# Optimization experiments

Hardware: AMD Instinct MI355X
Metric: run time of the kernel (lower is better)

The kernel has to match this reference:

```python
import jax, jax.numpy as jnp
import numpy as np

DIST_THRESHOLD = 0.1  # distance_threshold from __init__
NO_CODE_ID = -1


def setup_inputs() -> dict:
    key = jax.random.key(0)
    k1, k2 = jax.random.split(key)
    x = jax.random.normal(k1, (16, 4096, 64), dtype=jnp.float32)
    codes = jax.random.normal(k2, (4096, 64), dtype=jnp.float32)  # active codebook rows
    return {"x": x, "codes": codes}


def reference(x, codes):
    # Squared Euclidean distance (cdist ** 2) via the expansion
    x2 = jnp.sum(x * x, axis=-1, keepdims=True)            # [B, N, 1]
    c2 = jnp.sum(codes * codes, axis=-1)                    # [M]
    d2 = x2 + c2 - 2.0 * jnp.einsum("bnd,md->bnm", x, codes)  # [B, N, M]
    within = jnp.any(d2 <= DIST_THRESHOLD, axis=-1)         # [B, N]
    nn_ids = jnp.argmin(d2, axis=-1)                        # [B, N]
    return jnp.where(within, nn_ids, NO_CODE_ID)
```

## Files before the change

### kernel.cpp

```cpp
#include <hip/hip_runtime.h>
#include <stdint.h>

typedef float f32x4 __attribute__((ext_vector_type(4)));
typedef __bf16 bf16x8 __attribute__((ext_vector_type(8)));
typedef __bf16 bf16x4 __attribute__((ext_vector_type(4)));

#define NROWS 65536
#define NCODES 4096
#define NDIM 64
#define NSPLIT 4
#define STEPS 32
#define SSTEP 2
#define PHASES (STEPS / SSTEP)
#define BIAS 2048.0f
#define STRIPE_BYTES 131072u
#define STRIPE_MASK 0x1FFFFu


__device__ __forceinline__ void gld_lds16(const void* g, void* l) {
  __builtin_amdgcn_global_load_lds(
      (const __attribute__((address_space(1))) unsigned int*)g,
      (__attribute__((address_space(3))) unsigned int*)l, 16, 0, 0);
}

__device__ __forceinline__ uint32_t umin2(uint32_t a, uint32_t b) {
  return a < b ? a : b;
}

__global__ __launch_bounds__(256) void prep_codes_k(const float* __restrict__ codes,
                                                    float* __restrict__ nc2p,
                                                    __bf16* __restrict__ cb) {
  const int t = blockIdx.x * 256 + threadIdx.x;
  f32x4 v = *(const f32x4*)(codes + t * 4);
  bf16x4 o;
  float s = 0.f;
#pragma unroll
  for (int j = 0; j < 4; j++) {
    o[j] = (__bf16)v[j];
    s += v[j] * v[j];
  }
  *(bf16x4*)(cb + t * 4) = o;
  s += __shfl_xor(s, 1);
  s += __shfl_xor(s, 2);
  s += __shfl_xor(s, 4);
  s += __shfl_xor(s, 8);
  if ((threadIdx.x & 15) == 0) {
    const int c = t >> 4;
    const int pidx = (c >> 10) * 512 + ((c >> 5) & 31) * 16 + (c & 15);
    const int half = (c >> 4) & 1;
    nc2p[pidx * 2 + half] = -0.5f * s - BIAS;
  }
}

__global__ __launch_bounds__(256, 6) void nn_main(const float* __restrict__ x,
                                                  const __bf16* __restrict__ cbv,
                                                  const float2* __restrict__ nc2p,
                                                  uint32_t* __restrict__ karr,
                                                  float* __restrict__ x2arr) {
  const int tid  = threadIdx.x;
  const int lane = tid & 63;
  const int w    = tid >> 6;
  const int col  = lane & 15;
  const int quad = lane >> 4;
  const int stripe = blockIdx.x >> 9;
  const int rowgrp = blockIdx.x & 511;
  const int rowbase = rowgrp * 128 + w * 32;
  const int s0 = rowgrp & 31;
  const char* cbb = (const char*)cbv;

  __shared__ __align__(16) char stage[2][SSTEP * 4096];
  __shared__ __align__(8) float2 ncl[512];

  const uint32_t schunk = ((uint32_t)(tid * 16)) ^ ((((uint32_t)tid >> 3) & 7u) << 4);
  const char* srcbase = cbb + (uint32_t)stripe * STRIPE_BYTES + schunk;
  const uint32_t rot = (uint32_t)s0 * 4096u;
  gld_lds16((const char*)nc2p + stripe * 4096 + tid * 16, (char*)ncl + w * 1024);
#pragma unroll
  for (int i = 0; i < SSTEP; i++)
    gld_lds16(srcbase + ((rot + i * 4096u) & STRIPE_MASK),
              &stage[0][i * 4096 + w * 1024]);

  bf16x8 a[2][2];
  float x2part[2];
#pragma unroll
  for (int rt = 0; rt < 2; rt++) {
    const float* xr = x + (rowbase + rt * 16 + col) * NDIM + quad * 8;
    float p = 0.f;
#pragma unroll
    for (int kc = 0; kc < 2; kc++) {
      f32x4 v0 = *(const f32x4*)(xr + kc * 32);
      f32x4 v1 = *(const f32x4*)(xr + kc * 32 + 4);
      bf16x8 af;
#pragma unroll
      for (int j = 0; j < 4; j++) {
        af[j]     = (__bf16)v0[j];
        af[j + 4] = (__bf16)v1[j];
        p += v0[j] * v0[j] + v1[j] * v1[j];
      }
      a[rt][kc] = af;
    }
    x2part[rt] = p;
  }
#pragma unroll
  for (int rt = 0; rt < 2; rt++) {
    float p = x2part[rt];
    p += __shfl_xor(p, 16);
    p += __shfl_xor(p, 32);
    x2part[rt] = p;
  }
  if (stripe == 0 && quad == 0) {
#pragma unroll
    for (int rt = 0; rt < 2; rt++) x2arr[rowbase + rt * 16 + col] = x2part[rt];
  }

  uint32_t bestK[2][4];
#pragma unroll
  for (int rt = 0; rt < 2; rt++)
#pragma unroll
    for (int j = 0; j < 4; j++) bestK[rt][j] = 0xFFFFFFFFu;

  const uint32_t swz = ((uint32_t)(col & 7)) << 4;
  const uint32_t o00 = ((uint32_t)(col * 128 + quad * 16)) ^ swz;
  const uint32_t o01 = ((uint32_t)(col * 128 + 64 + quad * 16)) ^ swz;
  const uint32_t o10 = ((uint32_t)(2048 + col * 128 + quad * 16)) ^ swz;
  const uint32_t o11 = ((uint32_t)(2048 + col * 128 + 64 + quad * 16)) ^ swz;

  __syncthreads();

#pragma unroll 1
  for (int p = 0; p < PHASES; ++p) {
    if (p < PHASES - 1) {
      const uint32_t pb = rot + (uint32_t)(p + 1) * (SSTEP * 4096u);
      char* dst = &stage[(p + 1) & 1][w * 1024];
#pragma unroll
      for (int i = 0; i < SSTEP; i++)
        gld_lds16(srcbase + ((pb + i * 4096u) & STRIPE_MASK), dst + i * 4096);
    }
    const char* sb = stage[p & 1];
#pragma unroll
    for (int ss = 0; ss < SSTEP; ss++) {
      const int s_eff = (s0 + p * SSTEP + ss) & 31;
      const float2 nv = ncl[s_eff * 16 + col];
      bf16x8 b00 = *(const bf16x8*)(sb + ss * 4096 + o00);
      bf16x8 b01 = *(const bf16x8*)(sb + ss * 4096 + o01);
      bf16x8 b10 = *(const bf16x8*)(sb + ss * 4096 + o10);
      bf16x8 b11 = *(const bf16x8*)(sb + ss * 4096 + o11);
      f32x4 ci0 = {nv.x, nv.x, nv.x, nv.x};
      f32x4 ci1 = {nv.y, nv.y, nv.y, nv.y};
      const uint32_t vk0 = (uint32_t)(col | (s_eff << 5));
      const uint32_t vk1 = vk0 | 16u;
#pragma unroll
      for (int rt = 0; rt < 2; rt++) {
        f32x4 acc0 = __builtin_amdgcn_mfma_f32_16x16x32_bf16(a[rt][0], b00, ci0, 0, 0, 0);
        acc0 = __builtin_amdgcn_mfma_f32_16x16x32_bf16(a[rt][1], b01, acc0, 0, 0, 0);
        f32x4 acc1 = __builtin_amdgcn_mfma_f32_16x16x32_bf16(a[rt][0], b10, ci1, 0, 0, 0);
        acc1 = __builtin_amdgcn_mfma_f32_16x16x32_bf16(a[rt][1], b11, acc1, 0, 0, 0);
#pragma unroll
        for (int j = 0; j < 4; j++) {
          const uint32_t k0 = (__builtin_bit_cast(uint32_t, acc0[j]) & 0xFFFFFC00u) | vk0;
          const uint32_t k1 = (__builtin_bit_cast(uint32_t, acc1[j]) & 0xFFFFFC00u) | vk1;
          bestK[rt][j] = umin2(bestK[rt][j], umin2(k0, k1));
        }
      }
    }
    __syncthreads();
  }

#pragma unroll
  for (int rt = 0; rt < 2; rt++) {
#pragma unroll
    for (int j = 0; j < 4; j++) {
      uint32_t bk = bestK[rt][j];
#pragma unroll
      for (int off = 1; off < 16; off <<= 1) {
        const uint32_t ok = (uint32_t)__shfl_xor((int)bk, off);
        bk = umin2(bk, ok);
      }
      if (col == 0) {
        const int row = rowbase + rt * 16 + quad * 4 + j;
        karr[stripe * NROWS + row] = bk;
      }
    }
  }
}

__global__ __launch_bounds__(256) void nn_final(const uint32_t* __restrict__ karr,
                                                const float* __restrict__ x2arr,
                                                int* __restrict__ out) {
  const int row = blockIdx.x * blockDim.x + threadIdx.x;
  if (row >= NROWS) return;
  uint32_t best = karr[row];
  int bs = 0;
#pragma unroll
  for (int s = 1; s < NSPLIT; s++) {
    const uint32_t kk = karr[s * NROWS + row];
    if (kk < best) {
      best = kk;
      bs = s;
    }
  }
  const float Tp = __builtin_bit_cast(float, best & 0xFFFFFC00u);
  const float d2 = fmaf(-2.0f, Tp, x2arr[row]) - 2.0f * BIAS;
  out[row] = (d2 <= 0.1f) ? (bs * 1024 + (int)(best & 1023u)) : -1;
}

extern "C" void kernel_launch(void* const* d_in, const int* in_sizes, int n_in,
                              void* d_out, int out_size, void* d_ws, size_t ws_size,
                              hipStream_t stream) {
  const float* x = (const float*)d_in[0];
  const float* codes = (const float*)d_in[1];
  int* out = (int*)d_out;

  char* ws = (char*)d_ws;
  __bf16* cb = (__bf16*)ws;
  float* nc2p = (float*)(ws + 0x080000);
  uint32_t* karr = (uint32_t*)(ws + 0x100000);
  float* x2arr = (float*)(ws + 0x300000);

  prep_codes_k<<<256, 256, 0, stream>>>(codes, nc2p, cb);
  nn_main<<<2048, 256, 0, stream>>>(x, cb, (const float2*)nc2p, karr, x2arr);
  nn_final<<<256, 256, 0, stream>>>(karr, x2arr, out);
}
```

Baseline: 98.63 us.

## Drop codebook split across blocks and fuse final reduction into main kernel

Each block now scans all 4096 codes instead of one of four 1024-code stripes, so the grid shrinks from 2048 to 512 blocks. The threshold test and output write move into the main kernel, which removes the nn_final launch and the karr/x2arr workspace round trip. The packed key now keeps 12 index bits, so 2 fewer distance mantissa bits survive, slightly coarsening tie-breaking. With 512 blocks of 256 threads there may be too little parallelism to fill the GPU, and each block runs a loop four times longer.

Result: no change. 99.28 us (+0.7%).

```diff
diff --git a/kernel.cpp b/kernel.cpp
--- a/kernel.cpp
+++ b/kernel.cpp
@@ -8,13 +8,11 @@
 #define NROWS 65536
 #define NCODES 4096
 #define NDIM 64
-#define NSPLIT 4
-#define STEPS 32
+#define STEPS 128
 #define SSTEP 2
 #define PHASES (STEPS / SSTEP)
 #define BIAS 2048.0f
-#define STRIPE_BYTES 131072u
-#define STRIPE_MASK 0x1FFFFu
+#define CBMASK 0x7FFFF
 
 
 __device__ __forceinline__ void gld_lds16(const void* g, void* l) {
@@ -46,7 +44,7 @@
   s += __shfl_xor(s, 8);
   if ((threadIdx.x & 15) == 0) {
     const int c = t >> 4;
-    const int pidx = (c >> 10) * 512 + ((c >> 5) & 31) * 16 + (c & 15);
+    const int pidx = (c >> 5) * 16 + (c & 15);
     const int half = (c >> 4) & 1;
     nc2p[pidx * 2 + half] = -0.5f * s - BIAS;
   }
@@ -55,29 +53,30 @@
 __global__ __launch_bounds__(256, 6) void nn_main(const float* __restrict__ x,
                                                   const __bf16* __restrict__ cbv,
                                                   const float2* __restrict__ nc2p,
-                                                  uint32_t* __restrict__ karr,
-                                                  float* __restrict__ x2arr) {
+                                                  int* __restrict__ out) {
   const int tid  = threadIdx.x;
   const int lane = tid & 63;
   const int w    = tid >> 6;
   const int col  = lane & 15;
   const int quad = lane >> 4;
-  const int stripe = blockIdx.x >> 9;
-  const int rowgrp = blockIdx.x & 511;
-  const int rowbase = rowgrp * 128 + w * 32;
-  const int s0 = rowgrp & 31;
+  const int bid  = blockIdx.x;
+  const int rowbase = bid * 128 + w * 32;
+  const int s0 = bid & 127;
   const char* cbb = (const char*)cbv;
 
   __shared__ __align__(16) char stage[2][SSTEP * 4096];
-  __shared__ __align__(8) float2 ncl[512];
+  __shared__ __align__(8) float2 ncl[2048];
 
   const uint32_t schunk = ((uint32_t)(tid * 16)) ^ ((((uint32_t)tid >> 3) & 7u) << 4);
-  const char* srcbase = cbb + (uint32_t)stripe * STRIPE_BYTES + schunk;
+  const char* srcbase = cbb + schunk;
   const uint32_t rot = (uint32_t)s0 * 4096u;
-  gld_lds16((const char*)nc2p + stripe * 4096 + tid * 16, (char*)ncl + w * 1024);
+#pragma unroll
+  for (int i = 0; i < 4; i++)
+    gld_lds16((const char*)nc2p + i * 4096 + tid * 16,
+              (char*)ncl + i * 4096 + w * 1024);
 #pragma unroll
   for (int i = 0; i < SSTEP; i++)
-    gld_lds16(srcbase + ((rot + i * 4096u) & STRIPE_MASK),
+    gld_lds16(srcbase + ((rot + i * 4096u) & CBMASK),
               &stage[0][i * 4096 + w * 1024]);
 
   bf16x8 a[2][2];
@@ -108,10 +107,6 @@
     p += __shfl_xor(p, 32);
     x2part[rt] = p;
   }
-  if (stripe == 0 && quad == 0) {
-#pragma unroll
-    for (int rt = 0; rt < 2; rt++) x2arr[rowbase + rt * 16 + col] = x2part[rt];
-  }
 
   uint32_t bestK[2][4];
 #pragma unroll
@@ -134,12 +129,12 @@
       char* dst = &stage[(p + 1) & 1][w * 1024];
 #pragma unroll
       for (int i = 0; i < SSTEP; i++)
-        gld_lds16(srcbase + ((pb + i * 4096u) & STRIPE_MASK), dst + i * 4096);
+        gld_lds16(srcbase + ((pb + i * 4096u) & CBMASK), dst + i * 4096);
     }
     const char* sb = stage[p & 1];
 #pragma unroll
     for (int ss = 0; ss < SSTEP; ss++) {
-      const int s_eff = (s0 + p * SSTEP + ss) & 31;
+      const int s_eff = (s0 + p * SSTEP + ss) & 127;
       const float2 nv = ncl[s_eff * 16 + col];
       bf16x8 b00 = *(const bf16x8*)(sb + ss * 4096 + o00);
       bf16x8 b01 = *(const bf16x8*)(sb + ss * 4096 + o01);
@@ -157,8 +152,8 @@
         acc1 = __builtin_amdgcn_mfma_f32_16x16x32_bf16(a[rt][1], b11, acc1, 0, 0, 0);
 #pragma unroll
         for (int j = 0; j < 4; j++) {
-          const uint32_t k0 = (__builtin_bit_cast(uint32_t, acc0[j]) & 0xFFFFFC00u) | vk0;
-          const uint32_t k1 = (__builtin_bit_cast(uint32_t, acc1[j]) & 0xFFFFFC00u) | vk1;
+          const uint32_t k0 = (__builtin_bit_cast(uint32_t, acc0[j]) & 0xFFFFF000u) | vk0;
+          const uint32_t k1 = (__builtin_bit_cast(uint32_t, acc1[j]) & 0xFFFFF000u) | vk1;
           bestK[rt][j] = umin2(bestK[rt][j], umin2(k0, k1));
         }
       }
@@ -176,32 +171,15 @@
         const uint32_t ok = (uint32_t)__shfl_xor((int)bk, off);
         bk = umin2(bk, ok);
       }
+      const float x2v = __shfl(x2part[rt], (lane & 48) + quad * 4 + j);
       if (col == 0) {
-        const int row = rowbase + rt * 16 + quad * 4 + j;
-        karr[stripe * NROWS + row] = bk;
+        const float Tp = __builtin_bit_cast(float, bk & 0xFFFFF000u);
+        const float d2 = fmaf(-2.0f, Tp, x2v) - 2.0f * BIAS;
+        out[rowbase + rt * 16 + quad * 4 + j] =
+            (d2 <= 0.1f) ? (int)(bk & 4095u) : -1;
       }
     }
   }
-}
-
-__global__ __launch_bounds__(256) void nn_final(const uint32_t* __restrict__ karr,
-                                                const float* __restrict__ x2arr,
-                                                int* __restrict__ out) {
-  const int row = blockIdx.x * blockDim.x + threadIdx.x;
-  if (row >= NROWS) return;
-  uint32_t best = karr[row];
-  int bs = 0;
-#pragma unroll
-  for (int s = 1; s < NSPLIT; s++) {
-    const uint32_t kk = karr[s * NROWS + row];
-    if (kk < best) {
-      best = kk;
-      bs = s;
-    }
-  }
-  const float Tp = __builtin_bit_cast(float, best & 0xFFFFFC00u);
-  const float d2 = fmaf(-2.0f, Tp, x2arr[row]) - 2.0f * BIAS;
-  out[row] = (d2 <= 0.1f) ? (bs * 1024 + (int)(best & 1023u)) : -1;
 }
 
 extern "C" void kernel_launch(void* const* d_in, const int* in_sizes, int n_in,
@@ -214,10 +192,7 @@
   char* ws = (char*)d_ws;
   __bf16* cb = (__bf16*)ws;
   float* nc2p = (float*)(ws + 0x080000);
-  uint32_t* karr = (uint32_t*)(ws + 0x100000);
-  float* x2arr = (float*)(ws + 0x300000);
 
   prep_codes_k<<<256, 256, 0, stream>>>(codes, nc2p, cb);
-  nn_main<<<2048, 256, 0, stream>>>(x, cb, (const float2*)nc2p, karr, x2arr);
-  nn_final<<<256, 256, 0, stream>>>(karr, x2arr, out);
+  nn_main<<<512, 256, 0, stream>>>(x, cb, (const float2*)nc2p, out);
 }
```
